# Kernel optimization log

Hardware: AMD Instinct MI355X
Metric: run time of the kernel (lower is better)

The kernel has to match this reference:

```python
import jax, jax.numpy as jnp
import numpy as np

N_NODES = 100000
N_EDGES = 3200000
D = 128


def setup_inputs() -> dict:
    key = jax.random.key(0)
    k_feat, k_src, k_dst, k_w1, k_w2 = jax.random.split(key, 5)
    feat = jax.random.normal(k_feat, (N_NODES, D), dtype=jnp.float32)
    src = jax.random.randint(k_src, (N_EDGES,), 0, N_NODES, dtype=jnp.int32)
    dst = jax.random.randint(k_dst, (N_EDGES,), 0, N_NODES, dtype=jnp.int32)
    eps = jnp.zeros((1,), dtype=jnp.float32)
    s1 = 1.0 / np.sqrt(D)
    W1 = jax.random.normal(k_w1, (D, D), dtype=jnp.float32) * s1
    b1 = jnp.zeros((D,), dtype=jnp.float32)
    W2 = jax.random.normal(k_w2, (D, D), dtype=jnp.float32) * s1
    b2 = jnp.zeros((D,), dtype=jnp.float32)
    return {"feat": feat, "src": src, "dst": dst, "eps": eps,
            "W1": W1, "b1": b1, "W2": W2, "b2": b2}


def reference(feat, src, dst, eps, W1, b1, W2, b2):
    # message passing: copy source features along edges, sum-reduce at dst
    # neigh[v] = sum_{(u,v) in E} feat[u]
    msgs = feat[src]                                  # [E, D] gather
    neigh = jax.ops.segment_sum(msgs, dst, num_segments=feat.shape[0])  # [N, D]
    # GIN update: (1 + eps) * h_v + aggregated neighbors, then MLP
    h = (1.0 + eps[0]) * feat + neigh                 # [N, D]
    h = jax.nn.relu(h @ W1 + b1)                      # [N, D]
    out = h @ W2 + b2                                 # [N, D]
    return out
```

## Files before the change

### kernel.cpp

```cpp
#include <hip/hip_runtime.h>
#include <stdint.h>

#define N_NODES 100000
#define N_EDGES 3200000
#define DIM 128
#define NPAD 100032
#define NBINS 391
#define BCAP 10240
#define EPB 4096

typedef short short8 __attribute__((ext_vector_type(8)));
typedef float f32x4 __attribute__((ext_vector_type(4)));

__device__ __forceinline__ short f2bf(float x) {
    uint32_t u = __builtin_bit_cast(uint32_t, x);
    u += 0x7fffu + ((u >> 16) & 1u);
    return (short)(u >> 16);
}
__device__ __forceinline__ float bflo(uint32_t p) {
    return __builtin_bit_cast(float, p << 16);
}
__device__ __forceinline__ float bfhi(uint32_t p) {
    return __builtin_bit_cast(float, p & 0xffff0000u);
}
__device__ __forceinline__ uint32_t pack2(float x, float y) {
    return (uint32_t)(uint16_t)f2bf(x) | ((uint32_t)(uint16_t)f2bf(y) << 16);
}

__global__ __launch_bounds__(256) void prep_kernel(const float* __restrict__ feat,
                                                   uint32_t* __restrict__ featbf,
                                                   const float* __restrict__ w1,
                                                   const float* __restrict__ w2,
                                                   short* __restrict__ w1t,
                                                   short* __restrict__ w2t,
                                                   int* __restrict__ bincnt) {
    int b = blockIdx.x, t = threadIdx.x;
    if (b < 12500) {
        int i = b * 256 + t;
        float4 f = ((const float4*)feat)[i];
        featbf[2 * i]     = pack2(f.x, f.y);
        featbf[2 * i + 1] = pack2(f.z, f.w);
    } else if (b < 12564) {
        int i = (b - 12500) * 256 + t;
        int k = i >> 7, n = i & 127;
        w1t[n * DIM + k] = f2bf(w1[i]);
        w2t[n * DIM + k] = f2bf(w2[i]);
    } else {
        int i = (b - 12564) * 256 + t;
        bincnt[i] = 0;
    }
}

__global__ __launch_bounds__(256) void bin_kernel(const int* __restrict__ src,
                                                  const int* __restrict__ dst,
                                                  int* __restrict__ bincnt,
                                                  uint32_t* __restrict__ binpair) {
    __shared__ int hist[512];
    __shared__ int scanv[512];
    __shared__ int scan256[256];
    __shared__ int gbase[NBINS];
    __shared__ int cursor[NBINS];
    __shared__ uint32_t sorted[EPB];
    __shared__ int saddr[EPB];
    int t = threadIdx.x;
    for (int i = t; i < 512; i += 256) hist[i] = 0;
    __syncthreads();
    int e0 = blockIdx.x * EPB;
    int nn = min(EPB, N_EDGES - e0);
    int d[16];
#pragma unroll
    for (int i = 0; i < 16; i++) {
        int idx = i * 256 + t;
        d[i] = (idx < nn) ? dst[e0 + idx] : -1;
        if (d[i] >= 0) atomicAdd(&hist[d[i] >> 8], 1);
    }
    __syncthreads();
    int h0 = hist[2 * t], h1 = hist[2 * t + 1];
    scan256[t] = h0 + h1;
    __syncthreads();
    for (int dd = 1; dd < 256; dd <<= 1) {
        int v = (t >= dd) ? scan256[t - dd] : 0;
        __syncthreads();
        scan256[t] += v;
        __syncthreads();
    }
    int pairExcl = scan256[t] - (h0 + h1);
    scanv[2 * t] = pairExcl;
    scanv[2 * t + 1] = pairExcl + h0;
    for (int b = t; b < NBINS; b += 256) {
        int h = hist[b];
        gbase[b] = h ? atomicAdd(&bincnt[b], h) : 0;
        cursor[b] = 0;
    }
    __syncthreads();
#pragma unroll
    for (int i = 0; i < 16; i++) {
        if (d[i] >= 0) {
            int b = d[i] >> 8;
            int slot = atomicAdd(&cursor[b], 1);
            int p = scanv[b] + slot;
            int g = gbase[b] + slot;
            int e = e0 + i * 256 + t;
            sorted[p] = (uint32_t)src[e] | ((uint32_t)(d[i] & 255) << 24);
            saddr[p] = (g < BCAP) ? (b * BCAP + g) : -1;
        }
    }
    __syncthreads();
    for (int i = t; i < nn; i += 256) {
        int a = saddr[i];
        if (a >= 0) binpair[a] = sorted[i];
    }
}

__global__ __launch_bounds__(256) void csr_kernel(const int* __restrict__ bincnt,
                                                  const uint32_t* __restrict__ binpair,
                                                  int* __restrict__ rowptr,
                                                  int* __restrict__ csr) {
    __shared__ int hist[256];
    __shared__ int cursor[256];
    __shared__ int sc[256];
    __shared__ int binbase_s;
    int b = blockIdx.x;
    int t = threadIdx.x;
    int partial = 0;
    for (int j = t; j < b; j += 256) partial += min(bincnt[j], BCAP);
    sc[t] = partial;
    __syncthreads();
    for (int dd = 128; dd > 0; dd >>= 1) {
        if (t < dd) sc[t] += sc[t + dd];
        __syncthreads();
    }
    if (t == 0) binbase_s = sc[0];
    hist[t] = 0;
    __syncthreads();
    int binbase = binbase_s;
    int cntb = min(bincnt[b], BCAP);
    const uint32_t* pairs = binpair + (size_t)b * BCAP;
    for (int i = t; i < cntb; i += 256)
        atomicAdd(&hist[pairs[i] >> 24], 1);
    __syncthreads();
    int val = hist[t];
    sc[t] = val;
    __syncthreads();
    for (int dd = 1; dd < 256; dd <<= 1) {
        int addv = (t >= dd) ? sc[t - dd] : 0;
        __syncthreads();
        sc[t] += addv;
        __syncthreads();
    }
    int excl = sc[t] - val;
    rowptr[(b << 8) + t] = binbase + excl;
    cursor[t] = excl;
    __syncthreads();
    for (int i = t; i < cntb; i += 256) {
        uint32_t p = pairs[i];
        int s2 = atomicAdd(&cursor[p >> 24], 1);
        csr[binbase + s2] = (int)(p & 0x00FFFFFFu);
    }
}

#define ACC8(q) do { \
    a0 += bflo((q).x); a1 += bfhi((q).x); a2 += bflo((q).y); a3 += bfhi((q).y); \
    a4 += bflo((q).z); a5 += bfhi((q).z); a6 += bflo((q).w); a7 += bfhi((q).w); } while (0)

__global__ __launch_bounds__(256) void gather_kernel(const uint32_t* __restrict__ featbf,
                                                     const int* __restrict__ rowptr,
                                                     const int* __restrict__ csr,
                                                     const float* __restrict__ eps,
                                                     uint32_t* __restrict__ hbf) {
    int wid = blockIdx.x * 4 + (threadIdx.x >> 6);
    int lane = threadIdx.x & 63;
    int quarter = lane >> 4;
    int col = lane & 15;
    if (wid >= N_NODES) {
        if (wid < NPAD) hbf[wid * 64 + lane] = 0;
        return;
    }
    float e1 = 1.0f + eps[0];
    uint4 sf = *(const uint4*)&featbf[wid * 64 + col * 4];
    float a0 = 0.f, a1 = 0.f, a2 = 0.f, a3 = 0.f;
    float a4 = 0.f, a5 = 0.f, a6 = 0.f, a7 = 0.f;
    int start = rowptr[wid], end = rowptr[wid + 1];
    for (int base = start; base < end; base += 64) {
        int m = min(64, end - base);
        int u = (lane < m) ? csr[base + lane] : 0;
        int j = 0;
        for (; j + 32 <= m; j += 32) {
            int i0 = __shfl(u, j + quarter);
            int i1 = __shfl(u, j + 4 + quarter);
            int i2 = __shfl(u, j + 8 + quarter);
            int i3 = __shfl(u, j + 12 + quarter);
            int i4 = __shfl(u, j + 16 + quarter);
            int i5 = __shfl(u, j + 20 + quarter);
            int i6 = __shfl(u, j + 24 + quarter);
            int i7 = __shfl(u, j + 28 + quarter);
            uint4 q0 = *(const uint4*)&featbf[i0 * 64 + col * 4];
            uint4 q1 = *(const uint4*)&featbf[i1 * 64 + col * 4];
            uint4 q2 = *(const uint4*)&featbf[i2 * 64 + col * 4];
            uint4 q3 = *(const uint4*)&featbf[i3 * 64 + col * 4];
            uint4 q4 = *(const uint4*)&featbf[i4 * 64 + col * 4];
            uint4 q5 = *(const uint4*)&featbf[i5 * 64 + col * 4];
            uint4 q6 = *(const uint4*)&featbf[i6 * 64 + col * 4];
            uint4 q7 = *(const uint4*)&featbf[i7 * 64 + col * 4];
            ACC8(q0); ACC8(q1); ACC8(q2); ACC8(q3);
            ACC8(q4); ACC8(q5); ACC8(q6); ACC8(q7);
        }
        if (j < m) {
            int mm = m - 1;
            int p0 = j + quarter,      p1 = j + 4 + quarter;
            int p2 = j + 8 + quarter,  p3 = j + 12 + quarter;
            int p4 = j + 16 + quarter, p5 = j + 20 + quarter;
            int p6 = j + 24 + quarter, p7 = j + 28 + quarter;
            int i0 = __shfl(u, min(p0, mm)), i1 = __shfl(u, min(p1, mm));
            int i2 = __shfl(u, min(p2, mm)), i3 = __shfl(u, min(p3, mm));
            int i4 = __shfl(u, min(p4, mm)), i5 = __shfl(u, min(p5, mm));
            int i6 = __shfl(u, min(p6, mm)), i7 = __shfl(u, min(p7, mm));
            uint4 q0 = *(const uint4*)&featbf[i0 * 64 + col * 4];
            uint4 q1 = *(const uint4*)&featbf[i1 * 64 + col * 4];
            uint4 q2 = *(const uint4*)&featbf[i2 * 64 + col * 4];
            uint4 q3 = *(const uint4*)&featbf[i3 * 64 + col * 4];
            uint4 q4 = *(const uint4*)&featbf[i4 * 64 + col * 4];
            uint4 q5 = *(const uint4*)&featbf[i5 * 64 + col * 4];
            uint4 q6 = *(const uint4*)&featbf[i6 * 64 + col * 4];
            uint4 q7 = *(const uint4*)&featbf[i7 * 64 + col * 4];
            if (p0 < m) ACC8(q0);
            if (p1 < m) ACC8(q1);
            if (p2 < m) ACC8(q2);
            if (p3 < m) ACC8(q3);
            if (p4 < m) ACC8(q4);
            if (p5 < m) ACC8(q5);
            if (p6 < m) ACC8(q6);
            if (p7 < m) ACC8(q7);
        }
    }
    a0 += __shfl_xor(a0, 16); a1 += __shfl_xor(a1, 16);
    a2 += __shfl_xor(a2, 16); a3 += __shfl_xor(a3, 16);
    a4 += __shfl_xor(a4, 16); a5 += __shfl_xor(a5, 16);
    a6 += __shfl_xor(a6, 16); a7 += __shfl_xor(a7, 16);
    a0 += __shfl_xor(a0, 32); a1 += __shfl_xor(a1, 32);
    a2 += __shfl_xor(a2, 32); a3 += __shfl_xor(a3, 32);
    a4 += __shfl_xor(a4, 32); a5 += __shfl_xor(a5, 32);
    a6 += __shfl_xor(a6, 32); a7 += __shfl_xor(a7, 32);
    if (quarter == 0) {
        a0 += e1 * bflo(sf.x); a1 += e1 * bfhi(sf.x);
        a2 += e1 * bflo(sf.y); a3 += e1 * bfhi(sf.y);
        a4 += e1 * bflo(sf.z); a5 += e1 * bfhi(sf.z);
        a6 += e1 * bflo(sf.w); a7 += e1 * bfhi(sf.w);
        uint4 w;
        w.x = pack2(a0, a1); w.y = pack2(a2, a3);
        w.z = pack2(a4, a5); w.w = pack2(a6, a7);
        *(uint4*)&hbf[wid * 64 + col * 4] = w;
    }
}

__global__ __launch_bounds__(256) void mlp_kernel(const short* __restrict__ hbf,
                                                  const short* __restrict__ w1t,
                                                  const short* __restrict__ w2t,
                                                  const float* __restrict__ b1,
                                                  const float* __restrict__ b2,
                                                  float* __restrict__ out) {
    __shared__ __align__(16) short h1s[4][16 * 136];
    const int wave = threadIdx.x >> 6;
    const int lane = threadIdx.x & 63;
    const int l15 = lane & 15;
    const int quad = lane >> 4;

    float b1v[8], b2v[8];
#pragma unroll
    for (int n = 0; n < 8; n++) {
        b1v[n] = b1[n * 16 + l15];
        b2v[n] = b2[n * 16 + l15];
    }

    const int ntiles = NPAD / 64;
    for (int tile = blockIdx.x; tile < ntiles; tile += gridDim.x) {
        int row0 = tile * 64 + wave * 16;
        f32x4 acc[8];
#pragma unroll
        for (int n = 0; n < 8; n++) acc[n] = (f32x4){0.f, 0.f, 0.f, 0.f};
#pragma unroll
        for (int kb = 0; kb < DIM; kb += 32) {
            short8 a = *(const short8*)&hbf[(row0 + l15) * DIM + kb + quad * 8];
#pragma unroll
            for (int n = 0; n < 8; n++) {
                short8 b = *(const short8*)&w1t[(n * 16 + l15) * DIM + kb + quad * 8];
                acc[n] = __builtin_amdgcn_mfma_f32_16x16x32_bf16(a, b, acc[n], 0, 0, 0);
            }
        }
#pragma unroll
        for (int n = 0; n < 8; n++) {
#pragma unroll
            for (int r = 0; r < 4; r++) {
                float v = acc[n][r] + b1v[n];
                v = v > 0.f ? v : 0.f;
                h1s[wave][(quad * 4 + r) * 136 + n * 16 + l15] = f2bf(v);
            }
        }
        __syncthreads();
        f32x4 acc2[8];
#pragma unroll
        for (int n = 0; n < 8; n++) acc2[n] = (f32x4){0.f, 0.f, 0.f, 0.f};
#pragma unroll
        for (int kb = 0; kb < DIM; kb += 32) {
            short8 a2 = *(const short8*)&h1s[wave][l15 * 136 + kb + quad * 8];
#pragma unroll
            for (int n = 0; n < 8; n++) {
                short8 b = *(const short8*)&w2t[(n * 16 + l15) * DIM + kb + quad * 8];
                acc2[n] = __builtin_amdgcn_mfma_f32_16x16x32_bf16(a2, b, acc2[n], 0, 0, 0);
            }
        }
#pragma unroll
        for (int n = 0; n < 8; n++) {
#pragma unroll
            for (int r = 0; r < 4; r++) {
                int row = row0 + quad * 4 + r;
                if (row < N_NODES)
                    out[row * DIM + n * 16 + l15] = acc2[n][r] + b2v[n];
            }
        }
        __syncthreads();
    }
}

extern "C" void kernel_launch(void* const* d_in, const int* in_sizes, int n_in,
                              void* d_out, int out_size, void* d_ws, size_t ws_size,
                              hipStream_t stream) {
    const float* feat = (const float*)d_in[0];
    const int* src    = (const int*)d_in[1];
    const int* dst    = (const int*)d_in[2];
    const float* eps  = (const float*)d_in[3];
    const float* W1   = (const float*)d_in[4];
    const float* b1   = (const float*)d_in[5];
    const float* W2   = (const float*)d_in[6];
    const float* b2   = (const float*)d_in[7];
    float* out = (float*)d_out;

    char* ws = (char*)d_ws;
    int*      bincnt  = (int*)ws;
    int*      rowptr  = (int*)(ws + 2048);
    int*      csr     = (int*)(ws + 403456);
    uint32_t* binpair = (uint32_t*)(ws + 13203456);
    uint32_t* featbf  = (uint32_t*)(ws + 29218816);
    uint32_t* hbf     = (uint32_t*)(ws + 54818816);
    short*    w1t     = (short*)(ws + 80427008);
    short*    w2t     = (short*)(ws + 80459776);

    prep_kernel<<<12566, 256, 0, stream>>>(feat, featbf, W1, W2, w1t, w2t, bincnt);
    bin_kernel<<<(N_EDGES + EPB - 1) / EPB, 256, 0, stream>>>(src, dst, bincnt, binpair);
    csr_kernel<<<NBINS, 256, 0, stream>>>(bincnt, binpair, rowptr, csr);
    gather_kernel<<<NPAD / 4, 256, 0, stream>>>(featbf, rowptr, csr, eps, hbf);
    mlp_kernel<<<1563, 256, 0, stream>>>((const short*)hbf, w1t, w2t, b1, b2, out);
}
```

Baseline: 378.5 us.

## Stage CSR scatter in LDS, widen csr blocks, pack gather accumulators, split tail loads

csr_kernel now runs 1024 threads per bin and scatters sorted source indices into a shared-memory buffer, then writes them out to the csr array contiguously. This replaces random global scatter writes with coalesced ones. The gather kernel accumulates in float2 vectors, which may allow packed FP32 adds, and the remainder path issues only as many feature loads as it needs. The cost is about 40KB of LDS per block, which lowers occupancy in csr_kernel, plus extra branch code in the gather tail.

After: 363.8 us. 1.04x faster.

```diff
diff --git a/kernel.cpp b/kernel.cpp
--- a/kernel.cpp
+++ b/kernel.cpp
@@ -11,6 +11,7 @@
 
 typedef short short8 __attribute__((ext_vector_type(8)));
 typedef float f32x4 __attribute__((ext_vector_type(4)));
+typedef float f32x2 __attribute__((ext_vector_type(2)));
 
 __device__ __forceinline__ short f2bf(float x) {
     uint32_t u = __builtin_bit_cast(uint32_t, x);
@@ -25,6 +26,9 @@
 }
 __device__ __forceinline__ uint32_t pack2(float x, float y) {
     return (uint32_t)(uint16_t)f2bf(x) | ((uint32_t)(uint16_t)f2bf(y) << 16);
+}
+__device__ __forceinline__ f32x2 up2(uint32_t p) {
+    return (f32x2){ bflo(p), bfhi(p) };
 }
 
 __global__ __launch_bounds__(256) void prep_kernel(const float* __restrict__ feat,
@@ -112,56 +116,64 @@
     }
 }
 
-__global__ __launch_bounds__(256) void csr_kernel(const int* __restrict__ bincnt,
-                                                  const uint32_t* __restrict__ binpair,
-                                                  int* __restrict__ rowptr,
-                                                  int* __restrict__ csr) {
+__global__ __launch_bounds__(1024) void csr_kernel(const int* __restrict__ bincnt,
+                                                   const uint32_t* __restrict__ binpair,
+                                                   int* __restrict__ rowptr,
+                                                   int* __restrict__ csr) {
     __shared__ int hist[256];
     __shared__ int cursor[256];
     __shared__ int sc[256];
+    __shared__ int red[256];
     __shared__ int binbase_s;
+    __shared__ int sorted_s[BCAP];
     int b = blockIdx.x;
     int t = threadIdx.x;
-    int partial = 0;
-    for (int j = t; j < b; j += 256) partial += min(bincnt[j], BCAP);
-    sc[t] = partial;
+    if (t < 256) {
+        int partial = 0;
+        for (int j = t; j < b; j += 256) partial += min(bincnt[j], BCAP);
+        red[t] = partial;
+        hist[t] = 0;
+    }
     __syncthreads();
     for (int dd = 128; dd > 0; dd >>= 1) {
-        if (t < dd) sc[t] += sc[t + dd];
-        __syncthreads();
-    }
-    if (t == 0) binbase_s = sc[0];
-    hist[t] = 0;
+        if (t < dd) red[t] += red[t + dd];
+        __syncthreads();
+    }
+    if (t == 0) binbase_s = red[0];
     __syncthreads();
     int binbase = binbase_s;
     int cntb = min(bincnt[b], BCAP);
     const uint32_t* pairs = binpair + (size_t)b * BCAP;
-    for (int i = t; i < cntb; i += 256)
+    for (int i = t; i < cntb; i += 1024)
         atomicAdd(&hist[pairs[i] >> 24], 1);
     __syncthreads();
-    int val = hist[t];
-    sc[t] = val;
+    int val = 0;
+    if (t < 256) { val = hist[t]; sc[t] = val; }
     __syncthreads();
     for (int dd = 1; dd < 256; dd <<= 1) {
-        int addv = (t >= dd) ? sc[t - dd] : 0;
-        __syncthreads();
-        sc[t] += addv;
-        __syncthreads();
-    }
-    int excl = sc[t] - val;
-    rowptr[(b << 8) + t] = binbase + excl;
-    cursor[t] = excl;
-    __syncthreads();
-    for (int i = t; i < cntb; i += 256) {
+        int addv = (t < 256 && t >= dd) ? sc[t - dd] : 0;
+        __syncthreads();
+        if (t < 256) sc[t] += addv;
+        __syncthreads();
+    }
+    if (t < 256) {
+        int excl = sc[t] - val;
+        rowptr[(b << 8) + t] = binbase + excl;
+        cursor[t] = excl;
+    }
+    __syncthreads();
+    for (int i = t; i < cntb; i += 1024) {
         uint32_t p = pairs[i];
         int s2 = atomicAdd(&cursor[p >> 24], 1);
-        csr[binbase + s2] = (int)(p & 0x00FFFFFFu);
-    }
+        sorted_s[s2] = (int)(p & 0x00FFFFFFu);
+    }
+    __syncthreads();
+    for (int i = t; i < cntb; i += 1024)
+        csr[binbase + i] = sorted_s[i];
 }
 
 #define ACC8(q) do { \
-    a0 += bflo((q).x); a1 += bfhi((q).x); a2 += bflo((q).y); a3 += bfhi((q).y); \
-    a4 += bflo((q).z); a5 += bfhi((q).z); a6 += bflo((q).w); a7 += bfhi((q).w); } while (0)
+    a01 += up2((q).x); a23 += up2((q).y); a45 += up2((q).z); a67 += up2((q).w); } while (0)
 
 __global__ __launch_bounds__(256) void gather_kernel(const uint32_t* __restrict__ featbf,
                                                      const int* __restrict__ rowptr,
@@ -178,8 +190,8 @@
     }
     float e1 = 1.0f + eps[0];
     uint4 sf = *(const uint4*)&featbf[wid * 64 + col * 4];
-    float a0 = 0.f, a1 = 0.f, a2 = 0.f, a3 = 0.f;
-    float a4 = 0.f, a5 = 0.f, a6 = 0.f, a7 = 0.f;
+    f32x2 a01 = (f32x2){0.f, 0.f}, a23 = (f32x2){0.f, 0.f};
+    f32x2 a45 = (f32x2){0.f, 0.f}, a67 = (f32x2){0.f, 0.f};
     int start = rowptr[wid], end = rowptr[wid + 1];
     for (int base = start; base < end; base += 64) {
         int m = min(64, end - base);
@@ -205,34 +217,61 @@
             ACC8(q0); ACC8(q1); ACC8(q2); ACC8(q3);
             ACC8(q4); ACC8(q5); ACC8(q6); ACC8(q7);
         }
-        if (j < m) {
+        int r = m - j;
+        if (r > 0) {
             int mm = m - 1;
-            int p0 = j + quarter,      p1 = j + 4 + quarter;
-            int p2 = j + 8 + quarter,  p3 = j + 12 + quarter;
-            int p4 = j + 16 + quarter, p5 = j + 20 + quarter;
-            int p6 = j + 24 + quarter, p7 = j + 28 + quarter;
-            int i0 = __shfl(u, min(p0, mm)), i1 = __shfl(u, min(p1, mm));
-            int i2 = __shfl(u, min(p2, mm)), i3 = __shfl(u, min(p3, mm));
-            int i4 = __shfl(u, min(p4, mm)), i5 = __shfl(u, min(p5, mm));
-            int i6 = __shfl(u, min(p6, mm)), i7 = __shfl(u, min(p7, mm));
-            uint4 q0 = *(const uint4*)&featbf[i0 * 64 + col * 4];
-            uint4 q1 = *(const uint4*)&featbf[i1 * 64 + col * 4];
-            uint4 q2 = *(const uint4*)&featbf[i2 * 64 + col * 4];
-            uint4 q3 = *(const uint4*)&featbf[i3 * 64 + col * 4];
-            uint4 q4 = *(const uint4*)&featbf[i4 * 64 + col * 4];
-            uint4 q5 = *(const uint4*)&featbf[i5 * 64 + col * 4];
-            uint4 q6 = *(const uint4*)&featbf[i6 * 64 + col * 4];
-            uint4 q7 = *(const uint4*)&featbf[i7 * 64 + col * 4];
-            if (p0 < m) ACC8(q0);
-            if (p1 < m) ACC8(q1);
-            if (p2 < m) ACC8(q2);
-            if (p3 < m) ACC8(q3);
-            if (p4 < m) ACC8(q4);
-            if (p5 < m) ACC8(q5);
-            if (p6 < m) ACC8(q6);
-            if (p7 < m) ACC8(q7);
-        }
-    }
+            if (r > 16) {
+                int i0 = __shfl(u, j + quarter);
+                int i1 = __shfl(u, j + 4 + quarter);
+                int i2 = __shfl(u, j + 8 + quarter);
+                int i3 = __shfl(u, j + 12 + quarter);
+                int p4 = j + 16 + quarter, p5 = j + 20 + quarter;
+                int p6 = j + 24 + quarter, p7 = j + 28 + quarter;
+                int i4 = __shfl(u, min(p4, mm)), i5 = __shfl(u, min(p5, mm));
+                int i6 = __shfl(u, min(p6, mm)), i7 = __shfl(u, min(p7, mm));
+                uint4 q0 = *(const uint4*)&featbf[i0 * 64 + col * 4];
+                uint4 q1 = *(const uint4*)&featbf[i1 * 64 + col * 4];
+                uint4 q2 = *(const uint4*)&featbf[i2 * 64 + col * 4];
+                uint4 q3 = *(const uint4*)&featbf[i3 * 64 + col * 4];
+                uint4 q4 = *(const uint4*)&featbf[i4 * 64 + col * 4];
+                uint4 q5 = *(const uint4*)&featbf[i5 * 64 + col * 4];
+                uint4 q6 = *(const uint4*)&featbf[i6 * 64 + col * 4];
+                uint4 q7 = *(const uint4*)&featbf[i7 * 64 + col * 4];
+                ACC8(q0); ACC8(q1); ACC8(q2); ACC8(q3);
+                if (p4 < m) ACC8(q4);
+                if (p5 < m) ACC8(q5);
+                if (p6 < m) ACC8(q6);
+                if (p7 < m) ACC8(q7);
+            } else if (r > 8) {
+                int i0 = __shfl(u, j + quarter);
+                int i1 = __shfl(u, j + 4 + quarter);
+                int p2 = j + 8 + quarter, p3 = j + 12 + quarter;
+                int i2 = __shfl(u, min(p2, mm)), i3 = __shfl(u, min(p3, mm));
+                uint4 q0 = *(const uint4*)&featbf[i0 * 64 + col * 4];
+                uint4 q1 = *(const uint4*)&featbf[i1 * 64 + col * 4];
+                uint4 q2 = *(const uint4*)&featbf[i2 * 64 + col * 4];
+                uint4 q3 = *(const uint4*)&featbf[i3 * 64 + col * 4];
+                ACC8(q0); ACC8(q1);
+                if (p2 < m) ACC8(q2);
+                if (p3 < m) ACC8(q3);
+            } else if (r > 4) {
+                int i0 = __shfl(u, j + quarter);
+                int p1 = j + 4 + quarter;
+                int i1 = __shfl(u, min(p1, mm));
+                uint4 q0 = *(const uint4*)&featbf[i0 * 64 + col * 4];
+                uint4 q1 = *(const uint4*)&featbf[i1 * 64 + col * 4];
+                ACC8(q0);
+                if (p1 < m) ACC8(q1);
+            } else {
+                int p0 = j + quarter;
+                int i0 = __shfl(u, min(p0, mm));
+                uint4 q0 = *(const uint4*)&featbf[i0 * 64 + col * 4];
+                if (p0 < m) ACC8(q0);
+            }
+        }
+    }
+    float a0 = a01.x, a1 = a01.y, a2 = a23.x, a3 = a23.y;
+    float a4 = a45.x, a5 = a45.y, a6 = a67.x, a7 = a67.y;
     a0 += __shfl_xor(a0, 16); a1 += __shfl_xor(a1, 16);
     a2 += __shfl_xor(a2, 16); a3 += __shfl_xor(a3, 16);
     a4 += __shfl_xor(a4, 16); a5 += __shfl_xor(a5, 16);
@@ -347,7 +386,7 @@
 
     prep_kernel<<<12566, 256, 0, stream>>>(feat, featbf, W1, W2, w1t, w2t, bincnt);
     bin_kernel<<<(N_EDGES + EPB - 1) / EPB, 256, 0, stream>>>(src, dst, bincnt, binpair);
-    csr_kernel<<<NBINS, 256, 0, stream>>>(bincnt, binpair, rowptr, csr);
+    csr_kernel<<<NBINS, 1024, 0, stream>>>(bincnt, binpair, rowptr, csr);
     gather_kernel<<<NPAD / 4, 256, 0, stream>>>(featbf, rowptr, csr, eps, hbf);
     mlp_kernel<<<1563, 256, 0, stream>>>((const short*)hbf, w1t, w2t, b1, b2, out);
 }
```
